# Kernel tuning notes

Hardware: AMD Instinct MI355X
Metric: run time of the kernel (lower is better)

Reference implementation:

```python
import jax, jax.numpy as jnp
import numpy as np

B, S, D, H = 2, 2048, 1024, 16
HD = D // H  # head_dim = 64


def setup_inputs() -> dict:
    key = jax.random.key(0)
    ks = jax.random.split(key, 5)
    scale = 1.0 / np.sqrt(D)
    return {
        "x": jax.random.normal(ks[0], (B, S, D), dtype=jnp.float32),
        "w_qkv": jax.random.normal(ks[1], (D, 3 * D), dtype=jnp.float32) * scale,
        "b_qkv": jnp.zeros((3 * D,), dtype=jnp.float32),
        "w_out": jax.random.normal(ks[2], (D, D), dtype=jnp.float32) * scale,
        "b_out": jnp.zeros((D,), dtype=jnp.float32),
    }


def reference(x, w_qkv, b_qkv, w_out, b_out):
    b, s, d = x.shape
    qkv = x @ w_qkv + b_qkv  # [B,S,3D]
    q, k, v = jnp.split(qkv, 3, axis=-1)
    # [B,S,D] -> [B,H,S,HD]
    def to_heads(t):
        return t.reshape(b, s, H, HD).transpose(0, 2, 1, 3)
    q, k, v = to_heads(q), to_heads(k), to_heads(v)
    scores = jnp.einsum("bhqd,bhkd->bhqk", q, k) / np.sqrt(HD)
    attn = jax.nn.softmax(scores, axis=-1)
    out = jnp.einsum("bhqk,bhkd->bhqd", attn, v)  # [B,H,S,HD]
    out = out.transpose(0, 2, 1, 3).reshape(b, s, d)
    return out @ w_out + b_out
```

## Files before the change

### kernel.cpp

```cpp
#include <hip/hip_runtime.h>
#include <hip/hip_bf16.h>
#include <math.h>


typedef __bf16 bf16;
typedef __attribute__((ext_vector_type(8))) __bf16 bf16x8;
typedef __attribute__((ext_vector_type(4))) __bf16 bf16x4;
typedef __attribute__((ext_vector_type(4))) float f32x4;

#define B_ 2
#define S_ 2048
#define D_ 1024
#define H_ 16
#define HD_ 64

__device__ __forceinline__ f32x4 mfma16(bf16x8 a, bf16x8 b, f32x4 c) {
    return __builtin_amdgcn_mfma_f32_16x16x32_bf16(a, b, c, 0, 0, 0);
}

__device__ __forceinline__ void gload_lds16(const void* g, void* l) {
    __builtin_amdgcn_global_load_lds(
        (const __attribute__((address_space(1))) void*)g,
        (__attribute__((address_space(3))) void*)l, 16, 0, 0);
}


__global__ __launch_bounds__(256) void convert_x_kernel(
        const float* __restrict__ x, bf16* __restrict__ xb) {
    int i = blockIdx.x * 256 + threadIdx.x;
    float4 v = ((const float4*)x)[i];
    bf16x4 o = { (bf16)v.x, (bf16)v.y, (bf16)v.z, (bf16)v.w };
    ((bf16x4*)xb)[i] = o;
}

__global__ __launch_bounds__(256) void transpose_w_kernel(
        const float* __restrict__ src, bf16* __restrict__ dst, int K, int N) {
    __shared__ bf16 Ls[64 * 65];
    const int t = threadIdx.x;
    const int n0 = blockIdx.x * 64, k0 = blockIdx.y * 64;
    for (int p = 0; p < 4; p++) {
        int r = p * 16 + (t >> 4);
        int c4 = (t & 15) * 4;
        float4 v = *(const float4*)&src[(size_t)(k0 + r) * N + n0 + c4];
        Ls[r * 65 + c4 + 0] = (bf16)v.x;
        Ls[r * 65 + c4 + 1] = (bf16)v.y;
        Ls[r * 65 + c4 + 2] = (bf16)v.z;
        Ls[r * 65 + c4 + 3] = (bf16)v.w;
    }
    __syncthreads();
    for (int p = 0; p < 4; p++) {
        int nl = p * 16 + (t >> 4);
        int kc = (t & 15) * 4;
        bf16x4 o = { Ls[(kc + 0) * 65 + nl], Ls[(kc + 1) * 65 + nl],
                     Ls[(kc + 2) * 65 + nl], Ls[(kc + 3) * 65 + nl] };
        *(bf16x4*)&dst[(size_t)(n0 + nl) * K + k0 + kc] = o;
    }
}

template <bool OUT_BF16>
__global__ __launch_bounds__(256) void gemm_bt_kernel(
        const bf16* __restrict__ A, const bf16* __restrict__ Bt,
        const float* __restrict__ bias, void* __restrict__ Cout,
        int M, int N, int K) {
    __shared__ bf16 As[128 * 32];
    __shared__ bf16 Bs[128 * 32];
    const int t = threadIdx.x;
    const int lane = t & 63, w = t >> 6;
    const int g = lane >> 4, c = lane & 15;
    const int m0 = blockIdx.y * 128, n0 = blockIdx.x * 128;
    const int wm = (w >> 1) * 64, wn = (w & 1) * 64;

    f32x4 acc[4][4];
    for (int i = 0; i < 4; i++)
        for (int j = 0; j < 4; j++) acc[i][j] = (f32x4){0.f, 0.f, 0.f, 0.f};

    const size_t rowB = (size_t)K * 2;
    const char* Abase = (const char*)A + (size_t)m0 * rowB;
    const char* Bbase = (const char*)Bt + (size_t)n0 * rowB;

    for (int kt = 0; kt < K; kt += 32) {
        for (int i = 0; i < 2; i++) {
            int boff = (w * 2 + i) * 1024 + lane * 16;
            int row = boff >> 6;
            int colb = boff & 63;
            gload_lds16(Abase + (size_t)row * rowB + (size_t)kt * 2 + colb,
                        (char*)As + (w * 2 + i) * 1024);
            gload_lds16(Bbase + (size_t)row * rowB + (size_t)kt * 2 + colb,
                        (char*)Bs + (w * 2 + i) * 1024);
        }
        __syncthreads();
        bf16x8 af[4], bfr[4];
        for (int mt = 0; mt < 4; mt++)
            af[mt] = *(const bf16x8*)&As[(wm + mt * 16 + c) * 32 + g * 8];
        for (int nt = 0; nt < 4; nt++)
            bfr[nt] = *(const bf16x8*)&Bs[(wn + nt * 16 + c) * 32 + g * 8];
        for (int mt = 0; mt < 4; mt++)
            for (int nt = 0; nt < 4; nt++)
                acc[mt][nt] = mfma16(af[mt], bfr[nt], acc[mt][nt]);
        __syncthreads();
    }

    for (int mt = 0; mt < 4; mt++) {
        for (int nt = 0; nt < 4; nt++) {
            int col = n0 + wn + nt * 16 + c;
            float bv = bias[col];
            for (int r = 0; r < 4; r++) {
                int row = m0 + wm + mt * 16 + g * 4 + r;
                float v = acc[mt][nt][r] + bv;
                if (OUT_BF16)
                    ((bf16*)Cout)[(size_t)row * N + col] = (bf16)v;
                else
                    ((float*)Cout)[(size_t)row * N + col] = v;
            }
        }
    }
}

__global__ __launch_bounds__(256) void repack_v_kernel(
        const bf16* __restrict__ qkv, bf16* __restrict__ vt) {
    int bh = blockIdx.y, b = bh >> 4, h = bh & 15;
    int s0 = blockIdx.x * 64;
    int lane = threadIdx.x & 63, wv = threadIdx.x >> 6;
    int s = s0 + lane;
    const bf16* src = qkv + (size_t)(b * S_ + s) * (3 * D_) + 2 * D_ + h * HD_;
    bf16* dst = vt + (size_t)bh * HD_ * S_ + s;
    for (int i = 0; i < 16; i++) {
        int hd = wv * 16 + i;
        dst[(size_t)hd * S_] = src[hd];
    }
}

#define KT_ 64

__global__ __launch_bounds__(256) void attn_kernel(
        const bf16* __restrict__ qkv, const bf16* __restrict__ vt,
        bf16* __restrict__ out) {
    __shared__ bf16 Ks[2][KT_ * HD_];
    __shared__ bf16 Vs[2][HD_ * KT_];

    const int t = threadIdx.x;
    const int lane = t & 63, wv = t >> 6;
    const int g = lane >> 4, c = lane & 15;
    const int bh = blockIdx.y, b = bh >> 4, h = bh & 15;
    const int qbase = blockIdx.x * 128 + wv * 16;

    const float cs = 0.125f * 1.44269504088896341f;

    bf16x8 qf[2][2];
    for (int ch = 0; ch < 2; ch++) {
        const size_t qoff = (size_t)(b * S_ + qbase + ch * 64 + c) * (3 * D_) + h * HD_;
        qf[ch][0] = *(const bf16x8*)(qkv + qoff + g * 8);
        qf[ch][1] = *(const bf16x8*)(qkv + qoff + 32 + g * 8);
    }

    f32x4 o[2][4];
    for (int ch = 0; ch < 2; ch++)
        for (int i = 0; i < 4; i++) o[ch][i] = (f32x4){0.f, 0.f, 0.f, 0.f};
    f32x4 lsum[2];
    lsum[0] = lsum[1] = (f32x4){0.f, 0.f, 0.f, 0.f};

    size_t koff[2], voff[2];
    for (int j = 0; j < 2; j++) {
        int r = wv * 16 + j * 8 + (lane >> 3);
        int key = ((r >> 5) & 1) * 32 + ((r >> 3) & 1) * 16 +
                  ((r >> 2) & 1) * 8 + ((r >> 4) & 1) * 4 + (r & 3);
        int blk = (lane & 7) ^ (r & 7);
        koff[j] = (size_t)key * (3 * D_) + blk * 8;
        voff[j] = (size_t)r * S_ + blk * 8;
    }
    const bf16* kbase = qkv + (size_t)(b * S_) * (3 * D_) + D_ + h * HD_;
    const bf16* vbase = vt + (size_t)bh * HD_ * S_;

    for (int j = 0; j < 2; j++) {
        gload_lds16(kbase + koff[j], (char*)&Ks[0][0] + (wv * 2 + j) * 1024);
        gload_lds16(vbase + voff[j], (char*)&Vs[0][0] + (wv * 2 + j) * 1024);
    }
    __syncthreads();

    const int cs7 = c & 7;
    for (int tile = 0; tile < S_ / KT_; tile++) {
        const int buf = tile & 1;
        if (tile + 1 < S_ / KT_) {
            const int j0 = (tile + 1) * KT_;
            for (int j = 0; j < 2; j++) {
                gload_lds16(kbase + (size_t)j0 * (3 * D_) + koff[j],
                            (char*)&Ks[buf ^ 1][0] + (wv * 2 + j) * 1024);
                gload_lds16(vbase + j0 + voff[j],
                            (char*)&Vs[buf ^ 1][0] + (wv * 2 + j) * 1024);
            }
        }

        bf16x8 kf0[4], kf1[4];
        for (int kt = 0; kt < 4; kt++) {
            const bf16* row = &Ks[buf][(kt * 16 + c) * 64];
            kf0[kt] = *(const bf16x8*)(row + ((g ^ cs7) * 8));
            kf1[kt] = *(const bf16x8*)(row + (((g ^ 4) ^ cs7) * 8));
        }
        bf16x8 vf0[4], vf1[4];
        for (int nt = 0; nt < 4; nt++) {
            const bf16* row = &Vs[buf][(nt * 16 + c) * 64];
            vf0[nt] = *(const bf16x8*)(row + ((g ^ cs7) * 8));
            vf1[nt] = *(const bf16x8*)(row + (((g ^ 4) ^ cs7) * 8));
        }

        for (int ch = 0; ch < 2; ch++) {
            f32x4 p[4];
            for (int kt = 0; kt < 4; kt++) {
                f32x4 acc = (f32x4){0.f, 0.f, 0.f, 0.f};
                acc = mfma16(kf0[kt], qf[ch][0], acc);
                acc = mfma16(kf1[kt], qf[ch][1], acc);
                for (int r = 0; r < 4; r++)
                    p[kt][r] = __builtin_amdgcn_exp2f(acc[r] * cs);
            }
            lsum[ch] += (p[0] + p[1]) + (p[2] + p[3]);

            bf16x8 pb0, pb1;
            for (int r = 0; r < 4; r++) {
                pb0[r]     = (bf16)p[0][r];
                pb0[4 + r] = (bf16)p[1][r];
                pb1[r]     = (bf16)p[2][r];
                pb1[4 + r] = (bf16)p[3][r];
            }

            for (int nt = 0; nt < 4; nt++) {
                o[ch][nt] = mfma16(vf0[nt], pb0, o[ch][nt]);
                o[ch][nt] = mfma16(vf1[nt], pb1, o[ch][nt]);
            }
        }
        __syncthreads();
    }

    for (int ch = 0; ch < 2; ch++) {
        float lh = (lsum[ch][0] + lsum[ch][1]) + (lsum[ch][2] + lsum[ch][3]);
        lh += __shfl_xor(lh, 16);
        lh += __shfl_xor(lh, 32);
        float inv = 1.f / lh;
        int q = qbase + ch * 64 + c;
        size_t base = (size_t)(b * S_ + q) * D_ + h * HD_ + g * 4;
        for (int nt = 0; nt < 4; nt++) {
            bf16x4 ov = { (bf16)(o[ch][nt][0] * inv), (bf16)(o[ch][nt][1] * inv),
                          (bf16)(o[ch][nt][2] * inv), (bf16)(o[ch][nt][3] * inv) };
            *(bf16x4*)&out[base + nt * 16] = ov;
        }
    }
}


extern "C" void kernel_launch(void* const* d_in, const int* in_sizes, int n_in,
                              void* d_out, int out_size, void* d_ws, size_t ws_size,
                              hipStream_t stream) {
    const float* x     = (const float*)d_in[0];
    const float* w_qkv = (const float*)d_in[1];
    const float* b_qkv = (const float*)d_in[2];
    const float* w_out = (const float*)d_in[3];
    const float* b_out = (const float*)d_in[4];
    float* out = (float*)d_out;

    char* ws = (char*)d_ws;
    bf16* x_bf    = (bf16*)(ws + 0);
    bf16* attn_bf = x_bf;
    bf16* wqkv_t  = (bf16*)(ws + (8u << 20));
    bf16* wout_t  = (bf16*)(ws + (14u << 20));
    bf16* qkv_bf  = (bf16*)(ws + (16u << 20));
    bf16* v_t     = (bf16*)(ws + (40u << 20));

    convert_x_kernel<<<(B_ * S_ * D_) / (256 * 4), 256, 0, stream>>>(x, x_bf);
    transpose_w_kernel<<<dim3(3 * D_ / 64, D_ / 64), 256, 0, stream>>>(w_qkv, wqkv_t, D_, 3 * D_);
    transpose_w_kernel<<<dim3(D_ / 64, D_ / 64), 256, 0, stream>>>(w_out, wout_t, D_, D_);

    gemm_bt_kernel<true><<<dim3(3 * D_ / 128, B_ * S_ / 128), 256, 0, stream>>>(
        x_bf, wqkv_t, b_qkv, qkv_bf, B_ * S_, 3 * D_, D_);

    repack_v_kernel<<<dim3(S_ / 64, B_ * H_), 256, 0, stream>>>(qkv_bf, v_t);

    attn_kernel<<<dim3(S_ / 128, B_ * H_), 256, 0, stream>>>(qkv_bf, v_t, attn_bf);

    gemm_bt_kernel<false><<<dim3(D_ / 128, B_ * S_ / 128), 256, 0, stream>>>(
        attn_bf, wout_t, b_out, out, B_ * S_, D_, D_);
}
```

Before: 204.7 us.

## Split attention keys across two wave groups and fold softmax scale into Q weights

The attention kernel now runs 512 threads per block, with two groups of four waves each handling half of the key range. The partial outputs and row sums are combined through shared memory at the end. The softmax scale and log2(e) factor are folded into the Q columns of the QKV weights and bias, which removes a multiply before each exp2. Row sums are computed with an MFMA against a ones vector instead of vector adds, and P is packed to bf16 with paired conversions. Together these aim to raise parallelism and occupancy in attention and to cut VALU work in the inner loop, at the cost of an extra reduction step, double the LDS use, and a bf16-rounded row sum.

```diff
diff --git a/kernel.cpp b/kernel.cpp
--- a/kernel.cpp
+++ b/kernel.cpp
@@ -22,6 +22,15 @@
     __builtin_amdgcn_global_load_lds(
         (const __attribute__((address_space(1))) void*)g,
         (__attribute__((address_space(3))) void*)l, 16, 0, 0);
+}
+
+__device__ __forceinline__ bf16x8 pack8(const f32x4 a, const f32x4 b) {
+    union { bf16x8 v; __hip_bfloat162 h[4]; } u;
+    u.h[0] = __float22bfloat162_rn(make_float2(a[0], a[1]));
+    u.h[1] = __float22bfloat162_rn(make_float2(a[2], a[3]));
+    u.h[2] = __float22bfloat162_rn(make_float2(b[0], b[1]));
+    u.h[3] = __float22bfloat162_rn(make_float2(b[2], b[3]));
+    return u.v;
 }
 
 
@@ -34,18 +43,20 @@
 }
 
 __global__ __launch_bounds__(256) void transpose_w_kernel(
-        const float* __restrict__ src, bf16* __restrict__ dst, int K, int N) {
+        const float* __restrict__ src, bf16* __restrict__ dst, int K, int N,
+        float scale, int scale_cols) {
     __shared__ bf16 Ls[64 * 65];
     const int t = threadIdx.x;
     const int n0 = blockIdx.x * 64, k0 = blockIdx.y * 64;
+    const float sc = (n0 < scale_cols) ? scale : 1.0f;
     for (int p = 0; p < 4; p++) {
         int r = p * 16 + (t >> 4);
         int c4 = (t & 15) * 4;
         float4 v = *(const float4*)&src[(size_t)(k0 + r) * N + n0 + c4];
-        Ls[r * 65 + c4 + 0] = (bf16)v.x;
-        Ls[r * 65 + c4 + 1] = (bf16)v.y;
-        Ls[r * 65 + c4 + 2] = (bf16)v.z;
-        Ls[r * 65 + c4 + 3] = (bf16)v.w;
+        Ls[r * 65 + c4 + 0] = (bf16)(v.x * sc);
+        Ls[r * 65 + c4 + 1] = (bf16)(v.y * sc);
+        Ls[r * 65 + c4 + 2] = (bf16)(v.z * sc);
+        Ls[r * 65 + c4 + 3] = (bf16)(v.w * sc);
     }
     __syncthreads();
     for (int p = 0; p < 4; p++) {
@@ -61,7 +72,7 @@
 __global__ __launch_bounds__(256) void gemm_bt_kernel(
         const bf16* __restrict__ A, const bf16* __restrict__ Bt,
         const float* __restrict__ bias, void* __restrict__ Cout,
-        int M, int N, int K) {
+        int M, int N, int K, float bias_scale, int bias_cols) {
     __shared__ bf16 As[128 * 32];
     __shared__ bf16 Bs[128 * 32];
     const int t = threadIdx.x;
@@ -100,10 +111,11 @@
         __syncthreads();
     }
 
+    const float bsc = (n0 < bias_cols) ? bias_scale : 1.0f;
     for (int mt = 0; mt < 4; mt++) {
         for (int nt = 0; nt < 4; nt++) {
             int col = n0 + wn + nt * 16 + c;
-            float bv = bias[col];
+            float bv = bias[col] * bsc;
             for (int r = 0; r < 4; r++) {
                 int row = m0 + wm + mt * 16 + g * 4 + r;
                 float v = acc[mt][nt][r] + bv;
@@ -131,20 +143,23 @@
 }
 
 #define KT_ 64
-
-__global__ __launch_bounds__(256) void attn_kernel(
+#define KEYS_HALF_ (S_ / 2)
+
+__global__ __launch_bounds__(512, 4) void attn_kernel(
         const bf16* __restrict__ qkv, const bf16* __restrict__ vt,
         bf16* __restrict__ out) {
-    __shared__ bf16 Ks[2][KT_ * HD_];
-    __shared__ bf16 Vs[2][HD_ * KT_];
+    __shared__ bf16 KV[2][2][2][KT_ * HD_];
+    __shared__ float Ls2[128];
 
     const int t = threadIdx.x;
     const int lane = t & 63, wv = t >> 6;
+    const int half = wv >> 2, wvl = wv & 3;
     const int g = lane >> 4, c = lane & 15;
     const int bh = blockIdx.y, b = bh >> 4, h = bh & 15;
-    const int qbase = blockIdx.x * 128 + wv * 16;
-
-    const float cs = 0.125f * 1.44269504088896341f;
+    const int qbase = blockIdx.x * 128 + wvl * 16;
+
+    const bf16 onev = (bf16)1.0f;
+    const bf16x8 ones = { onev, onev, onev, onev, onev, onev, onev, onev };
 
     bf16x8 qf[2][2];
     for (int ch = 0; ch < 2; ch++) {
@@ -156,49 +171,49 @@
     f32x4 o[2][4];
     for (int ch = 0; ch < 2; ch++)
         for (int i = 0; i < 4; i++) o[ch][i] = (f32x4){0.f, 0.f, 0.f, 0.f};
-    f32x4 lsum[2];
-    lsum[0] = lsum[1] = (f32x4){0.f, 0.f, 0.f, 0.f};
+    f32x4 lacc[2];
+    lacc[0] = lacc[1] = (f32x4){0.f, 0.f, 0.f, 0.f};
 
     size_t koff[2], voff[2];
     for (int j = 0; j < 2; j++) {
-        int r = wv * 16 + j * 8 + (lane >> 3);
+        int r = wvl * 16 + j * 8 + (lane >> 3);
         int key = ((r >> 5) & 1) * 32 + ((r >> 3) & 1) * 16 +
                   ((r >> 2) & 1) * 8 + ((r >> 4) & 1) * 4 + (r & 3);
         int blk = (lane & 7) ^ (r & 7);
         koff[j] = (size_t)key * (3 * D_) + blk * 8;
         voff[j] = (size_t)r * S_ + blk * 8;
     }
-    const bf16* kbase = qkv + (size_t)(b * S_) * (3 * D_) + D_ + h * HD_;
-    const bf16* vbase = vt + (size_t)bh * HD_ * S_;
+    const bf16* kbase = qkv + (size_t)(b * S_ + half * KEYS_HALF_) * (3 * D_) + D_ + h * HD_;
+    const bf16* vbase = vt + (size_t)bh * HD_ * S_ + half * KEYS_HALF_;
 
     for (int j = 0; j < 2; j++) {
-        gload_lds16(kbase + koff[j], (char*)&Ks[0][0] + (wv * 2 + j) * 1024);
-        gload_lds16(vbase + voff[j], (char*)&Vs[0][0] + (wv * 2 + j) * 1024);
+        gload_lds16(kbase + koff[j], (char*)&KV[half][0][0][0] + (wvl * 2 + j) * 1024);
+        gload_lds16(vbase + voff[j], (char*)&KV[half][1][0][0] + (wvl * 2 + j) * 1024);
     }
     __syncthreads();
 
     const int cs7 = c & 7;
-    for (int tile = 0; tile < S_ / KT_; tile++) {
+    for (int tile = 0; tile < KEYS_HALF_ / KT_; tile++) {
         const int buf = tile & 1;
-        if (tile + 1 < S_ / KT_) {
+        if (tile + 1 < KEYS_HALF_ / KT_) {
             const int j0 = (tile + 1) * KT_;
             for (int j = 0; j < 2; j++) {
                 gload_lds16(kbase + (size_t)j0 * (3 * D_) + koff[j],
-                            (char*)&Ks[buf ^ 1][0] + (wv * 2 + j) * 1024);
+                            (char*)&KV[half][0][buf ^ 1][0] + (wvl * 2 + j) * 1024);
                 gload_lds16(vbase + j0 + voff[j],
-                            (char*)&Vs[buf ^ 1][0] + (wv * 2 + j) * 1024);
+                            (char*)&KV[half][1][buf ^ 1][0] + (wvl * 2 + j) * 1024);
             }
         }
 
         bf16x8 kf0[4], kf1[4];
         for (int kt = 0; kt < 4; kt++) {
-            const bf16* row = &Ks[buf][(kt * 16 + c) * 64];
+            const bf16* row = &KV[half][0][buf][(kt * 16 + c) * 64];
             kf0[kt] = *(const bf16x8*)(row + ((g ^ cs7) * 8));
             kf1[kt] = *(const bf16x8*)(row + (((g ^ 4) ^ cs7) * 8));
         }
         bf16x8 vf0[4], vf1[4];
         for (int nt = 0; nt < 4; nt++) {
-            const bf16* row = &Vs[buf][(nt * 16 + c) * 64];
+            const bf16* row = &KV[half][1][buf][(nt * 16 + c) * 64];
             vf0[nt] = *(const bf16x8*)(row + ((g ^ cs7) * 8));
             vf1[nt] = *(const bf16x8*)(row + (((g ^ 4) ^ cs7) * 8));
         }
@@ -210,17 +225,14 @@
                 acc = mfma16(kf0[kt], qf[ch][0], acc);
                 acc = mfma16(kf1[kt], qf[ch][1], acc);
                 for (int r = 0; r < 4; r++)
-                    p[kt][r] = __builtin_amdgcn_exp2f(acc[r] * cs);
-            }
-            lsum[ch] += (p[0] + p[1]) + (p[2] + p[3]);
-
-            bf16x8 pb0, pb1;
-            for (int r = 0; r < 4; r++) {
-                pb0[r]     = (bf16)p[0][r];
-                pb0[4 + r] = (bf16)p[1][r];
-                pb1[r]     = (bf16)p[2][r];
-                pb1[4 + r] = (bf16)p[3][r];
-            }
+                    p[kt][r] = __builtin_amdgcn_exp2f(acc[r]);
+            }
+
+            bf16x8 pb0 = pack8(p[0], p[1]);
+            bf16x8 pb1 = pack8(p[2], p[3]);
+
+            lacc[ch] = mfma16(ones, pb0, lacc[ch]);
+            lacc[ch] = mfma16(ones, pb1, lacc[ch]);
 
             for (int nt = 0; nt < 4; nt++) {
                 o[ch][nt] = mfma16(vf0[nt], pb0, o[ch][nt]);
@@ -230,17 +242,30 @@
         __syncthreads();
     }
 
-    for (int ch = 0; ch < 2; ch++) {
-        float lh = (lsum[ch][0] + lsum[ch][1]) + (lsum[ch][2] + lsum[ch][3]);
-        lh += __shfl_xor(lh, 16);
-        lh += __shfl_xor(lh, 32);
-        float inv = 1.f / lh;
-        int q = qbase + ch * 64 + c;
-        size_t base = (size_t)(b * S_ + q) * D_ + h * HD_ + g * 4;
-        for (int nt = 0; nt < 4; nt++) {
-            bf16x4 ov = { (bf16)(o[ch][nt][0] * inv), (bf16)(o[ch][nt][1] * inv),
-                          (bf16)(o[ch][nt][2] * inv), (bf16)(o[ch][nt][3] * inv) };
-            *(bf16x4*)&out[base + nt * 16] = ov;
+    float* Os = (float*)&KV[1][0][0][0];
+    if (half == 1) {
+        for (int ch = 0; ch < 2; ch++) {
+            for (int nt = 0; nt < 4; nt++)
+                *(f32x4*)&Os[(((wvl * 2 + ch) * 4 + nt) * 64 + lane) * 4] = o[ch][nt];
+            if (lane < 16)
+                Ls2[ch * 64 + wvl * 16 + c] = lacc[ch][0];
+        }
+    }
+    __syncthreads();
+    if (half == 0) {
+        for (int ch = 0; ch < 2; ch++) {
+            float lh = lacc[ch][0] + Ls2[ch * 64 + wvl * 16 + c];
+            float inv = 1.f / lh;
+            int q = qbase + ch * 64 + c;
+            size_t base = (size_t)(b * S_ + q) * D_ + h * HD_ + g * 4;
+            for (int nt = 0; nt < 4; nt++) {
+                f32x4 po = *(const f32x4*)&Os[(((wvl * 2 + ch) * 4 + nt) * 64 + lane) * 4];
+                bf16x4 ov = { (bf16)((o[ch][nt][0] + po[0]) * inv),
+                              (bf16)((o[ch][nt][1] + po[1]) * inv),
+                              (bf16)((o[ch][nt][2] + po[2]) * inv),
+                              (bf16)((o[ch][nt][3] + po[3]) * inv) };
+                *(bf16x4*)&out[base + nt * 16] = ov;
+            }
         }
     }
 }
@@ -256,6 +281,8 @@
     const float* b_out = (const float*)d_in[4];
     float* out = (float*)d_out;
 
+    const float cs = 0.125f * 1.44269504088896341f;
+
     char* ws = (char*)d_ws;
     bf16* x_bf    = (bf16*)(ws + 0);
     bf16* attn_bf = x_bf;
@@ -265,16 +292,18 @@
     bf16* v_t     = (bf16*)(ws + (40u << 20));
 
     convert_x_kernel<<<(B_ * S_ * D_) / (256 * 4), 256, 0, stream>>>(x, x_bf);
-    transpose_w_kernel<<<dim3(3 * D_ / 64, D_ / 64), 256, 0, stream>>>(w_qkv, wqkv_t, D_, 3 * D_);
-    transpose_w_kernel<<<dim3(D_ / 64, D_ / 64), 256, 0, stream>>>(w_out, wout_t, D_, D_);
+    transpose_w_kernel<<<dim3(3 * D_ / 64, D_ / 64), 256, 0, stream>>>(
+        w_qkv, wqkv_t, D_, 3 * D_, cs, D_);
+    transpose_w_kernel<<<dim3(D_ / 64, D_ / 64), 256, 0, stream>>>(
+        w_out, wout_t, D_, D_, 1.0f, 0);
 
     gemm_bt_kernel<true><<<dim3(3 * D_ / 128, B_ * S_ / 128), 256, 0, stream>>>(
-        x_bf, wqkv_t, b_qkv, qkv_bf, B_ * S_, 3 * D_, D_);
+        x_bf, wqkv_t, b_qkv, qkv_bf, B_ * S_, 3 * D_, D_, cs, D_);
 
     repack_v_kernel<<<dim3(S_ / 64, B_ * H_), 256, 0, stream>>>(qkv_bf, v_t);
 
-    attn_kernel<<<dim3(S_ / 128, B_ * H_), 256, 0, stream>>>(qkv_bf, v_t, attn_bf);
+    attn_kernel<<<dim3(S_ / 128, B_ * H_), 512, 0, stream>>>(qkv_bf, v_t, attn_bf);
 
     gemm_bt_kernel<false><<<dim3(D_ / 128, B_ * S_ / 128), 256, 0, stream>>>(
-        attn_bf, wout_t, b_out, out, B_ * S_, D_, D_);
-}
+        attn_bf, wout_t, b_out, out, B_ * S_, D_, D_, 1.0f, 0);
+}
```

Result: faster. 199.2 us (-2.7%).
